# Performance work log

Measured on AMD Instinct MI355X. Metric: run time of the kernel, lower is better.

The kernel has to match this reference:

```python
import jax, jax.numpy as jnp
import numpy as np

N0, N1, N2 = 100000, 25000, 6250
E0, E1, E2 = 600000, 150000, 37500
K = 6


def cheb_conv(x, edge_index, W, b):
    """torch_geometric ChebConv with sym normalization, lambda_max=2:
    L_hat = -D^{-1/2} A D^{-1/2}; T0=x, T1=L_hat x, Tk=2 L_hat T_{k-1} - T_{k-2}."""
    n = x.shape[0]
    src, dst = edge_index[0], edge_index[1]
    deg = jax.ops.segment_sum(jnp.ones(src.shape[0], x.dtype), src, num_segments=n)
    dinv = jnp.where(deg > 0, jax.lax.rsqrt(jnp.maximum(deg, 1.0)), 0.0)
    w = -(dinv[src] * dinv[dst])  # [E]

    def prop(h):  # (L_hat h)_i = sum_{j->i} w_ij h_j
        return jax.ops.segment_sum(w[:, None] * h[src], dst, num_segments=n)

    Tx0 = x
    out = Tx0 @ W[0]
    Tx1 = prop(x)
    out = out + Tx1 @ W[1]
    for k in range(2, W.shape[0]):
        Tx2 = 2.0 * prop(Tx1) - Tx0
        out = out + Tx2 @ W[k]
        Tx0, Tx1 = Tx1, Tx2
    return out + b


def pool(x, rows, cols, vals, n_out):
    # sparse.mm(D, x): y[r] += v * x[c]
    return jax.ops.segment_sum(vals[:, None] * x[cols], rows, num_segments=n_out)


def setup_inputs() -> dict:
    key = jax.random.key(0)
    ks = jax.random.split(key, 16)
    inp = {}
    inp["x"] = jax.random.normal(ks[0], (N0, 3), jnp.float32)
    inp["edge_index0"] = jax.random.randint(ks[1], (2, E0), 0, N0, jnp.int32)
    inp["edge_index1"] = jax.random.randint(ks[2], (2, E1), 0, N1, jnp.int32)
    inp["edge_index2"] = jax.random.randint(ks[3], (2, E2), 0, N2, jnp.int32)
    s = 0.05
    inp["W0"] = jax.random.normal(ks[4], (K, 3, 128), jnp.float32) * s
    inp["b0"] = jax.random.normal(ks[5], (128,), jnp.float32) * s
    inp["W1"] = jax.random.normal(ks[6], (K, 128, 128), jnp.float32) * s
    inp["b1"] = jax.random.normal(ks[7], (128,), jnp.float32) * s
    inp["W2"] = jax.random.normal(ks[8], (K, 128, 256), jnp.float32) * s
    inp["b2"] = jax.random.normal(ks[9], (256,), jnp.float32) * s
    inp["D0_rows"] = jax.random.randint(ks[10], (100000,), 0, N1, jnp.int32)
    inp["D0_cols"] = jax.random.randint(ks[11], (100000,), 0, N0, jnp.int32)
    inp["D0_vals"] = jax.random.uniform(ks[12], (100000,), jnp.float32)
    inp["D1_rows"] = jax.random.randint(ks[13], (25000,), 0, N2, jnp.int32)
    inp["D1_cols"] = jax.random.randint(ks[14], (25000,), 0, N1, jnp.int32)
    inp["D1_vals"] = jax.random.uniform(ks[15], (25000,), jnp.float32)
    k2 = jax.random.split(jax.random.fold_in(key, 1), 2)
    inp["linW"] = jax.random.normal(k2[0], (10, N2 * 256), jnp.float32) * 0.001
    inp["linb"] = jax.random.normal(k2[1], (10,), jnp.float32) * s
    return inp


def reference(x, edge_index0, edge_index1, edge_index2, W0, b0, W1, b1, W2, b2,
              D0_rows, D0_cols, D0_vals, D1_rows, D1_cols, D1_vals, linW, linb):
    h = jax.nn.relu(cheb_conv(x, edge_index0, W0, b0))      # [N0,128]
    h = pool(h, D0_rows, D0_cols, D0_vals, N1)               # [N1,128]
    h = jax.nn.relu(cheb_conv(h, edge_index1, W1, b1))      # [N1,128]
    h = pool(h, D1_rows, D1_cols, D1_vals, N2)               # [N2,128]
    h = cheb_conv(h, edge_index2, W2, b2)                    # [N2,256]
    Z = linW @ h.reshape(-1) + linb                           # [10]
    return Z
```

## Files before the change

kernel.cpp:

```cpp
#include <hip/hip_runtime.h>


namespace {
constexpr int cN0 = 100000, cN1 = 25000, cN2 = 6250;
constexpr int cE0 = 600000, cE1 = 150000, cE2 = 37500;
constexpr int cD  = cN2 * 256;

constexpr int JN[8]  = {cN0, cN1, cN2, cN1, cN2, cN0, cN1, cN2};
constexpr int JE[8]  = {cE0, cE1, cE2, 100000, 25000, cE0, cE1, cE2};
constexpr int JB[8]  = {391, 98, 25, 98, 25, 391, 98, 25};
constexpr int JBBASE[9] = {0, 391, 489, 514, 612, 637, 1028, 1126, 1151};
constexpr int TB = 1151;
constexpr int JCB[8] = {293, 74, 19, 49, 13, 293, 74, 19};
constexpr int JCBASE[9] = {0, 293, 367, 386, 435, 448, 741, 815, 834};
constexpr int TCB = 834;
constexpr int CHUNK = 2048;
constexpr int BSTRIDE = 400;

constexpr int EBASE[5]   = {0, 600000, 750000, 787500, 887500};
constexpr int E_TOTAL    = 912500;
constexpr int SBASE[3]   = {0, 600000, 750000};
constexpr int S_TOTAL    = 787500;
constexpr int NBASE[5]   = {0, 100096, 125184, 131584, 156672};
constexpr int NPAD_TOTAL = 163072;
constexpr int DEGBASE[3] = {0, 100000, 125000};
constexpr int DEG_TOTAL  = 131250;
}

typedef __attribute__((ext_vector_type(8))) short short8;
typedef __attribute__((ext_vector_type(4))) float floatx4;

__device__ inline ushort f2bf(float f) {
  union { float f; unsigned u; } v; v.f = f;
  unsigned u = v.u;
  return (ushort)((u + 0x7FFFu + ((u >> 16) & 1u)) >> 16);
}

__device__ inline int job_of_cb(int cb) {
  int j = 0;
  while (cb >= JCBASE[j + 1]) ++j;
  return j;
}
__device__ inline int job_of_bucket(int g) {
  int j = 0;
  while (g >= JBBASE[j + 1]) ++j;
  return j;
}

__global__ __launch_bounds__(256) void c1_count_kernel(
    const int* __restrict__ k0, const int* __restrict__ k1, const int* __restrict__ k2,
    const int* __restrict__ k3, const int* __restrict__ k4, const int* __restrict__ k5,
    const int* __restrict__ k6, const int* __restrict__ k7,
    int* __restrict__ cntCB) {
  __shared__ int cnt[BSTRIDE];
  int cb = blockIdx.x;
  int j = job_of_cb(cb);
  int lb = cb - JCBASE[j];
  const int* keys;
  switch (j) {
    case 0: keys = k0; break; case 1: keys = k1; break; case 2: keys = k2; break;
    case 3: keys = k3; break; case 4: keys = k4; break; case 5: keys = k5; break;
    case 6: keys = k6; break; default: keys = k7; break;
  }
  int nB = JB[j];
  for (int b = threadIdx.x; b < nB; b += 256) cnt[b] = 0;
  __syncthreads();
  int e0 = lb * CHUNK;
  int e1 = min(e0 + CHUNK, JE[j]);
  for (int e = e0 + threadIdx.x; e < e1; e += 256)
    atomicAdd(&cnt[keys[e] >> 8], 1);
  __syncthreads();
  for (int b = threadIdx.x; b < nB; b += 256)
    cntCB[cb * BSTRIDE + b] = cnt[b];
}

__global__ __launch_bounds__(256) void c2a_scan_kernel(int* __restrict__ cntCB,
                                                       int* __restrict__ bucketTot) {
  __shared__ int s[256];
  int g = blockIdx.x;
  int j = job_of_bucket(g);
  int b = g - JBBASE[j];
  int cb0 = JCBASE[j], nCB = JCB[j];
  int carry = 0;
  for (int c0 = 0; c0 < nCB; c0 += 256) {
    int i = c0 + threadIdx.x;
    int v = (i < nCB) ? cntCB[(cb0 + i) * BSTRIDE + b] : 0;
    s[threadIdx.x] = v;
    __syncthreads();
    for (int d = 1; d < 256; d <<= 1) {
      int t = (threadIdx.x >= d) ? s[threadIdx.x - d] : 0;
      __syncthreads();
      s[threadIdx.x] += t;
      __syncthreads();
    }
    if (i < nCB) cntCB[(cb0 + i) * BSTRIDE + b] = carry + s[threadIdx.x] - v;
    carry += s[255];
    __syncthreads();
  }
  if (threadIdx.x == 0) bucketTot[g] = carry;
}

__global__ __launch_bounds__(256) void c2b_scan_kernel(const int* __restrict__ bucketTot,
                                                       int* __restrict__ bucketBase) {
  __shared__ int s[256];
  int j = blockIdx.x;
  int g0 = JBBASE[j], nB = JB[j];
  int carry = 0;
  for (int c0 = 0; c0 < nB; c0 += 256) {
    int i = c0 + threadIdx.x;
    int v = (i < nB) ? bucketTot[g0 + i] : 0;
    s[threadIdx.x] = v;
    __syncthreads();
    for (int d = 1; d < 256; d <<= 1) {
      int t = (threadIdx.x >= d) ? s[threadIdx.x - d] : 0;
      __syncthreads();
      s[threadIdx.x] += t;
      __syncthreads();
    }
    if (i < nB) bucketBase[g0 + i] = carry + s[threadIdx.x] - v;
    carry += s[255];
    __syncthreads();
  }
}

__global__ __launch_bounds__(256) void c3_src_kernel(
    const int* __restrict__ s0, const int* __restrict__ s1, const int* __restrict__ s2,
    const int* __restrict__ cntCB, const int* __restrict__ bucketBase,
    int* __restrict__ scatSrc) {
  __shared__ int base[BSTRIDE];
  int cb = blockIdx.x + JCBASE[5];
  int j = job_of_cb(cb);
  int lb = cb - JCBASE[j];
  const int* keys = (j == 5) ? s0 : (j == 6) ? s1 : s2;
  int nB = JB[j];
  for (int b = threadIdx.x; b < nB; b += 256)
    base[b] = SBASE[j - 5] + bucketBase[JBBASE[j] + b] + cntCB[cb * BSTRIDE + b];
  __syncthreads();
  int e0 = lb * CHUNK;
  int e1 = min(e0 + CHUNK, JE[j]);
  for (int e = e0 + threadIdx.x; e < e1; e += 256) {
    int s = keys[e];
    int pos = atomicAdd(&base[s >> 8], 1);
    scatSrc[pos] = s & 255;
  }
}

__global__ __launch_bounds__(256) void ddeg_kernel(const int* __restrict__ scatSrc,
                                                   const int* __restrict__ bucketTot,
                                                   const int* __restrict__ bucketBase,
                                                   float* __restrict__ dinv) {
  __shared__ int cnt[256];
  int g = blockIdx.x + JBBASE[5];
  int j = job_of_bucket(g);
  int b = g - JBBASE[j];
  int st = SBASE[j - 5] + bucketBase[g];
  int en = st + bucketTot[g];
  cnt[threadIdx.x] = 0;
  __syncthreads();
  for (int idx = st + threadIdx.x; idx < en; idx += 256)
    atomicAdd(&cnt[scatSrc[idx]], 1);
  __syncthreads();
  int node = b * 256 + threadIdx.x;
  if (node < JN[j]) {
    int c = cnt[threadIdx.x];
    dinv[DEGBASE[j - 5] + node] = (c > 0) ? rsqrtf((float)c) : 0.f;
  }
}

__global__ __launch_bounds__(256) void c3_dst_kernel(
    const int* __restrict__ d0, const int* __restrict__ s0,
    const int* __restrict__ d1, const int* __restrict__ s1,
    const int* __restrict__ d2, const int* __restrict__ s2,
    const int* __restrict__ p0r, const int* __restrict__ p0c, const float* __restrict__ p0v,
    const int* __restrict__ p1r, const int* __restrict__ p1c, const float* __restrict__ p1v,
    const float* __restrict__ dinv,
    const int* __restrict__ cntCB, const int* __restrict__ bucketBase,
    int2* __restrict__ scatPairs) {
  __shared__ int base[BSTRIDE];
  int cb = blockIdx.x;
  int j = job_of_cb(cb);
  int lb = cb - JCBASE[j];
  const int* dk; const int* sk; const float* vv = nullptr;
  switch (j) {
    case 0: dk = d0; sk = s0; break;
    case 1: dk = d1; sk = s1; break;
    case 2: dk = d2; sk = s2; break;
    case 3: dk = p0r; sk = p0c; vv = p0v; break;
    default: dk = p1r; sk = p1c; vv = p1v; break;
  }
  int nB = JB[j];
  for (int b = threadIdx.x; b < nB; b += 256)
    base[b] = EBASE[j] + bucketBase[JBBASE[j] + b] + cntCB[cb * BSTRIDE + b];
  __syncthreads();
  int e0 = lb * CHUNK;
  int e1 = min(e0 + CHUNK, JE[j]);
  for (int e = e0 + threadIdx.x; e < e1; e += 256) {
    int d = dk[e];
    int s = sk[e];
    float w;
    if (j < 3) w = -(dinv[DEGBASE[j] + s] * dinv[DEGBASE[j] + d]);
    else w = vv[e];
    int pos = atomicAdd(&base[d >> 8], 1);
    scatPairs[pos] = make_int2(((d & 255) << 17) | s, __float_as_int(w));
  }
}

__global__ __launch_bounds__(256) void dcsr_kernel(const int2* __restrict__ scatPairs,
                                                   const int* __restrict__ bucketTot,
                                                   const int* __restrict__ bucketBase,
                                                   int* __restrict__ off,
                                                   int2* __restrict__ csrPairs) {
  __shared__ int cnt[256];
  __shared__ int sArr[256];
  __shared__ int cur[256];
  int g = blockIdx.x;
  int j = job_of_bucket(g);
  int b = g - JBBASE[j];
  int relBase = bucketBase[g];
  int st = EBASE[j] + relBase;
  int en = st + bucketTot[g];
  cnt[threadIdx.x] = 0;
  __syncthreads();
  for (int idx = st + threadIdx.x; idx < en; idx += 256)
    atomicAdd(&cnt[scatPairs[idx].x >> 17], 1);
  __syncthreads();
  int v = cnt[threadIdx.x];
  sArr[threadIdx.x] = v;
  __syncthreads();
  for (int d = 1; d < 256; d <<= 1) {
    int t = (threadIdx.x >= d) ? sArr[threadIdx.x - d] : 0;
    __syncthreads();
    sArr[threadIdx.x] += t;
    __syncthreads();
  }
  int excl = sArr[threadIdx.x] - v;
  int node = b * 256 + threadIdx.x;
  if (node < JN[j]) off[NBASE[j] + node] = relBase + excl;
  if (threadIdx.x == 0 && b == JB[j] - 1) off[NBASE[j] + JN[j]] = JE[j];
  cur[threadIdx.x] = st + excl;
  __syncthreads();
  for (int idx = st + threadIdx.x; idx < en; idx += 256) {
    int2 p = scatPairs[idx];
    int dl = p.x >> 17;
    int s = p.x & 0x1FFFF;
    int pos = atomicAdd(&cur[dl], 1);
    csrPairs[pos] = make_int2(s, p.y);
  }
}

__global__ __launch_bounds__(256) void csr_prop128_kernel(
    const int* __restrict__ off, const int2* __restrict__ pairs,
    const float* __restrict__ h, float* __restrict__ y, ushort* __restrict__ ybf,
    const float* __restrict__ prev, float scale, int N) {
  int r = blockIdx.x * 8 + (threadIdx.x >> 5);
  int l = threadIdx.x & 31;
  if (r >= N) return;
  int s = off[r], e = off[r + 1];
  const float4* h4 = (const float4*)h;
  float ax = 0.f, ay = 0.f, az = 0.f, aw = 0.f;
  int j = s;
  for (; j + 4 <= e; j += 4) {
    int2 p0 = pairs[j], p1 = pairs[j + 1], p2 = pairs[j + 2], p3 = pairs[j + 3];
    float4 v0 = h4[(size_t)p0.x * 32 + l];
    float4 v1 = h4[(size_t)p1.x * 32 + l];
    float4 v2 = h4[(size_t)p2.x * 32 + l];
    float4 v3 = h4[(size_t)p3.x * 32 + l];
    float w0 = __int_as_float(p0.y), w1 = __int_as_float(p1.y);
    float w2 = __int_as_float(p2.y), w3 = __int_as_float(p3.y);
    ax += w0 * v0.x + w1 * v1.x + w2 * v2.x + w3 * v3.x;
    ay += w0 * v0.y + w1 * v1.y + w2 * v2.y + w3 * v3.y;
    az += w0 * v0.z + w1 * v1.z + w2 * v2.z + w3 * v3.z;
    aw += w0 * v0.w + w1 * v1.w + w2 * v2.w + w3 * v3.w;
  }
  for (; j < e; ++j) {
    int2 p = pairs[j];
    float4 v0 = h4[(size_t)p.x * 32 + l];
    float w = __int_as_float(p.y);
    ax += w * v0.x; ay += w * v0.y; az += w * v0.z; aw += w * v0.w;
  }
  float4 v = make_float4(scale * ax, scale * ay, scale * az, scale * aw);
  if (prev) {
    float4 pv = ((const float4*)prev)[(size_t)r * 32 + l];
    v.x -= pv.x; v.y -= pv.y; v.z -= pv.z; v.w -= pv.w;
  }
  if (y) ((float4*)y)[(size_t)r * 32 + l] = v;
  uint2 sp = make_uint2(f2bf(v.x) | ((unsigned)f2bf(v.y) << 16),
                        f2bf(v.z) | ((unsigned)f2bf(v.w) << 16));
  ((uint2*)ybf)[(size_t)r * 32 + l] = sp;
}

__global__ void csr_prop3_kernel(const int* __restrict__ off, const int2* __restrict__ pairs,
                                 const float4* __restrict__ h, float4* __restrict__ y,
                                 const float4* __restrict__ prev, float scale, int N) {
  int r = blockIdx.x * blockDim.x + threadIdx.x;
  if (r >= N) return;
  int s = off[r], e = off[r + 1];
  float ax = 0.f, ay = 0.f, az = 0.f;
  int j = s;
  for (; j + 4 <= e; j += 4) {
    int2 p0 = pairs[j], p1 = pairs[j + 1], p2 = pairs[j + 2], p3 = pairs[j + 3];
    float4 h0 = h[p0.x], h1 = h[p1.x], h2 = h[p2.x], h3 = h[p3.x];
    float w0 = __int_as_float(p0.y), w1 = __int_as_float(p1.y);
    float w2 = __int_as_float(p2.y), w3 = __int_as_float(p3.y);
    ax += w0 * h0.x + w1 * h1.x + w2 * h2.x + w3 * h3.x;
    ay += w0 * h0.y + w1 * h1.y + w2 * h2.y + w3 * h3.y;
    az += w0 * h0.z + w1 * h1.z + w2 * h2.z + w3 * h3.z;
  }
  for (; j < e; ++j) {
    int2 p = pairs[j];
    float4 hv = h[p.x];
    float w = __int_as_float(p.y);
    ax += w * hv.x; ay += w * hv.y; az += w * hv.z;
  }
  float4 v = make_float4(scale * ax, scale * ay, scale * az, 0.f);
  if (prev) {
    float4 pv = prev[r];
    v.x -= pv.x; v.y -= pv.y; v.z -= pv.z;
  }
  y[r] = v;
}

__global__ void copyx_kernel(const float* __restrict__ x, float4* __restrict__ Tb, int N) {
  int r = blockIdx.x * 256 + threadIdx.x;
  if (r < N) Tb[r] = make_float4(x[3 * r], x[3 * r + 1], x[3 * r + 2], 0.f);
}

__global__ __launch_bounds__(256) void h0_kernel(
    const float4* __restrict__ Tb0, const float* __restrict__ W0,
    const float* __restrict__ b0, float* __restrict__ h0, int N0) {
  int r = blockIdx.x * 2 + (threadIdx.x >> 7);
  int f = threadIdx.x & 127;
  float wcol[18];
#pragma unroll
  for (int t = 0; t < 18; ++t) wcol[t] = W0[t * 128 + f];
  if (r >= N0) return;
  float d = b0[f];
#pragma unroll
  for (int k = 0; k < 6; ++k) {
    float4 t = Tb0[(size_t)k * N0 + r];
    d += t.x * wcol[k * 3] + t.y * wcol[k * 3 + 1] + t.z * wcol[k * 3 + 2];
  }
  h0[(size_t)r * 128 + f] = fmaxf(d, 0.f);
}

__global__ void prep_w_kernel(const float* __restrict__ W1, const float* __restrict__ W2,
                              ushort* __restrict__ Wt1, ushort* __restrict__ Wt2) {
  int i = blockIdx.x * 256 + threadIdx.x;
  if (i < 768 * 128) {
    int k = i / 128, n = i - k * 128;
    Wt1[(size_t)n * 768 + k] = f2bf(W1[i]);
  } else {
    int i2 = i - 768 * 128;
    if (i2 < 768 * 256) {
      int k = i2 / 256, n = i2 - k * 256;
      Wt2[(size_t)n * 768 + k] = f2bf(W2[i2]);
    }
  }
}

template <int RELU>
__global__ __launch_bounds__(256, 2) void gemm_mfma_kernel(
    const ushort* __restrict__ Tbf, const ushort* __restrict__ Wt,
    const float* __restrict__ bias, float* __restrict__ C, int M, int N) {
  __shared__ ushort Al[64][40];
  __shared__ ushort Bl[128][40];
  const int tid = threadIdx.x;
  const int rowBase = blockIdx.x * 64;
  const int colBase = blockIdx.y * 128;
  const int wave = tid >> 6;
  const int lane = tid & 63;
  const int m16 = lane & 15;
  const int quad = lane >> 4;
  const size_t Mstride = (size_t)M * 128;

  floatx4 acc[8];
#pragma unroll
  for (int c = 0; c < 8; ++c)
#pragma unroll
    for (int r = 0; r < 4; ++r) acc[c][r] = 0.f;

  const int sRow = tid >> 2;
  const int sK8 = (tid & 3) * 8;
  const int growA = rowBase + sRow;
  const bool aValid = growA < M;

  for (int kc = 0; kc < 24; ++kc) {
    uint4 av = make_uint4(0, 0, 0, 0);
    if (aValid)
      av = *(const uint4*)(Tbf + (size_t)(kc >> 2) * Mstride + (size_t)growA * 128
                           + ((kc & 3) << 5) + sK8);
    *(uint4*)&Al[sRow][sK8] = av;
#pragma unroll
    for (int l = 0; l < 2; ++l) {
      int lin = tid + l * 256;
      int bRow = lin >> 2;
      int bK8 = (lin & 3) * 8;
      *(uint4*)&Bl[bRow][bK8] =
          *(const uint4*)(Wt + (size_t)(colBase + bRow) * 768 + kc * 32 + bK8);
    }
    __syncthreads();

    short8 a = *(const short8*)&Al[wave * 16 + m16][quad * 8];
#pragma unroll
    for (int c = 0; c < 8; ++c) {
      short8 b = *(const short8*)&Bl[c * 16 + m16][quad * 8];
      acc[c] = __builtin_amdgcn_mfma_f32_16x16x32_bf16(a, b, acc[c], 0, 0, 0);
    }
    __syncthreads();
  }

#pragma unroll
  for (int c = 0; c < 8; ++c) {
    int col = colBase + c * 16 + m16;
    float bv = bias[col];
#pragma unroll
    for (int r = 0; r < 4; ++r) {
      int row = rowBase + wave * 16 + quad * 4 + r;
      if (row < M) {
        float v = acc[c][r] + bv;
        if (RELU) v = fmaxf(v, 0.f);
        C[(size_t)row * N + col] = v;
      }
    }
  }
}

__global__ void initout_kernel(float* __restrict__ out, const float* __restrict__ linb) {
  int i = threadIdx.x;
  if (i < 10) out[i] = linb[i];
}

__global__ __launch_bounds__(256) void linear_kernel(const float* __restrict__ Wl,
                                                     const float* __restrict__ h,
                                                     float* __restrict__ out, int D) {
  float p[10];
#pragma unroll
  for (int j = 0; j < 10; ++j) p[j] = 0.f;
  int stride = gridDim.x * blockDim.x;
  for (int i = blockIdx.x * blockDim.x + threadIdx.x; i < D; i += stride) {
    float hv = h[i];
#pragma unroll
    for (int j = 0; j < 10; ++j) p[j] += Wl[(size_t)j * D + i] * hv;
  }
#pragma unroll
  for (int j = 0; j < 10; ++j) {
#pragma unroll
    for (int off = 32; off > 0; off >>= 1) p[j] += __shfl_down(p[j], off, 64);
  }
  __shared__ float s[4][10];
  int wave = threadIdx.x >> 6, lane = threadIdx.x & 63;
  if (lane == 0) {
#pragma unroll
    for (int j = 0; j < 10; ++j) s[wave][j] = p[j];
  }
  __syncthreads();
  if (threadIdx.x < 10) {
    float t = s[0][threadIdx.x] + s[1][threadIdx.x] + s[2][threadIdx.x] + s[3][threadIdx.x];
    atomicAdd(&out[threadIdx.x], t);
  }
}

extern "C" void kernel_launch(void* const* d_in, const int* in_sizes, int n_in,
                              void* d_out, int out_size, void* d_ws, size_t ws_size,
                              hipStream_t stream) {
  const float* x    = (const float*)d_in[0];
  const int*   ei0  = (const int*)d_in[1];
  const int*   ei1  = (const int*)d_in[2];
  const int*   ei2  = (const int*)d_in[3];
  const float* W0   = (const float*)d_in[4];
  const float* b0   = (const float*)d_in[5];
  const float* W1   = (const float*)d_in[6];
  const float* b1   = (const float*)d_in[7];
  const float* W2   = (const float*)d_in[8];
  const float* b2   = (const float*)d_in[9];
  const int*   D0r  = (const int*)d_in[10];
  const int*   D0c  = (const int*)d_in[11];
  const float* D0v  = (const float*)d_in[12];
  const int*   D1r  = (const int*)d_in[13];
  const int*   D1c  = (const int*)d_in[14];
  const float* D1v  = (const float*)d_in[15];
  const float* linW = (const float*)d_in[16];
  const float* linb = (const float*)d_in[17];
  float* out = (float*)d_out;
  (void)in_sizes; (void)n_in; (void)out_size; (void)ws_size;

  const int* src0 = ei0;            const int* dst0 = ei0 + cE0;
  const int* src1 = ei1;            const int* dst1 = ei1 + cE1;
  const int* src2 = ei2;            const int* dst2 = ei2 + cE2;

  float* ws = (float*)d_ws;
  size_t off = 0;
  auto alloc = [&](size_t n) {
    float* p = ws + off;
    off += (n + 63) & ~size_t(63);
    return p;
  };
  float* dinv       = alloc(DEG_TOTAL);
  int*   cntCB      = (int*)alloc((size_t)TCB * BSTRIDE);
  int*   bucketTot  = (int*)alloc(TB);
  int*   bucketBase = (int*)alloc(TB);
  int*   scatSrc    = (int*)alloc(S_TOTAL);
  int2*  scatPairs  = (int2*)alloc((size_t)2 * E_TOTAL);
  int2*  csrPairs   = (int2*)alloc((size_t)2 * E_TOTAL);
  int*   offArr     = (int*)alloc(NPAD_TOTAL);
  ushort* Wt1       = (ushort*)alloc(768 * 128 / 2);
  ushort* Wt2       = (ushort*)alloc(768 * 256 / 2);
  float4* Tb0       = (float4*)alloc((size_t)6 * cN0 * 4);
  float* h0buf      = alloc((size_t)cN0 * 128);
  float* Tlvl1      = alloc((size_t)6 * cN1 * 128);
  ushort* Tbf1      = (ushort*)alloc((size_t)6 * cN1 * 64);
  float* out1       = alloc((size_t)cN1 * 128);
  float* Tlvl2      = alloc((size_t)6 * cN2 * 128);
  ushort* Tbf2      = (ushort*)alloc((size_t)6 * cN2 * 64);
  float* out2       = alloc((size_t)cN2 * 256);

  auto nb = [](long long n) { return (unsigned)((n + 255) / 256); };

  c1_count_kernel<<<TCB, 256, 0, stream>>>(dst0, dst1, dst2, D0r, D1r,
                                           src0, src1, src2, cntCB);
  c2a_scan_kernel<<<TB, 256, 0, stream>>>(cntCB, bucketTot);
  c2b_scan_kernel<<<8, 256, 0, stream>>>(bucketTot, bucketBase);
  c3_src_kernel<<<TCB - JCBASE[5], 256, 0, stream>>>(src0, src1, src2,
                                                     cntCB, bucketBase, scatSrc);
  ddeg_kernel<<<TB - JBBASE[5], 256, 0, stream>>>(scatSrc, bucketTot, bucketBase, dinv);
  c3_dst_kernel<<<JCBASE[5], 256, 0, stream>>>(dst0, src0, dst1, src1, dst2, src2,
                                               D0r, D0c, D0v, D1r, D1c, D1v,
                                               dinv, cntCB, bucketBase, scatPairs);
  dcsr_kernel<<<JBBASE[5], 256, 0, stream>>>(scatPairs, bucketTot, bucketBase,
                                             offArr, csrPairs);
  prep_w_kernel<<<nb(768 * 384), 256, 0, stream>>>(W1, W2, Wt1, Wt2);

  auto seg_off   = [&](int s) { return offArr + NBASE[s]; };
  auto seg_pairs = [&](int s) { return csrPairs + EBASE[s]; };

  copyx_kernel<<<nb(cN0), 256, 0, stream>>>(x, Tb0, cN0);
  {
    auto Tk = [&](int k) { return Tb0 + (size_t)k * cN0; };
    csr_prop3_kernel<<<nb(cN0), 256, 0, stream>>>(seg_off(0), seg_pairs(0),
        Tk(0), Tk(1), nullptr, 1.f, cN0);
    csr_prop3_kernel<<<nb(cN0), 256, 0, stream>>>(seg_off(0), seg_pairs(0),
        Tk(1), Tk(2), Tk(0), 2.f, cN0);
    csr_prop3_kernel<<<nb(cN0), 256, 0, stream>>>(seg_off(0), seg_pairs(0),
        Tk(2), Tk(3), Tk(1), 2.f, cN0);
    csr_prop3_kernel<<<nb(cN0), 256, 0, stream>>>(seg_off(0), seg_pairs(0),
        Tk(3), Tk(4), Tk(2), 2.f, cN0);
    csr_prop3_kernel<<<nb(cN0), 256, 0, stream>>>(seg_off(0), seg_pairs(0),
        Tk(4), Tk(5), Tk(3), 2.f, cN0);
  }
  h0_kernel<<<(cN0 + 1) / 2, 256, 0, stream>>>(Tb0, W0, b0, h0buf, cN0);
  csr_prop128_kernel<<<(cN1 + 7) / 8, 256, 0, stream>>>(
      seg_off(3), seg_pairs(3), h0buf, Tlvl1, Tbf1, nullptr, 1.f, cN1);

  {
    auto Tk  = [&](int k) { return Tlvl1 + (size_t)k * cN1 * 128; };
    auto Tbk = [&](int k) { return Tbf1 + (size_t)k * cN1 * 128; };
    auto prop = [&](int kin, int kout, int kprev, float scale, bool needF32) {
      csr_prop128_kernel<<<(cN1 + 7) / 8, 256, 0, stream>>>(
          seg_off(1), seg_pairs(1), Tk(kin), needF32 ? Tk(kout) : nullptr, Tbk(kout),
          (kprev >= 0) ? Tk(kprev) : nullptr, scale, cN1);
    };
    prop(0, 1, -1, 1.f, true);
    prop(1, 2, 0, 2.f, true);
    prop(2, 3, 1, 2.f, true);
    prop(3, 4, 2, 2.f, true);
    prop(4, 5, 3, 2.f, false);
    dim3 g((cN1 + 63) / 64, 1);
    gemm_mfma_kernel<1><<<g, 256, 0, stream>>>(Tbf1, Wt1, b1, out1, cN1, 128);
  }

  csr_prop128_kernel<<<(cN2 + 7) / 8, 256, 0, stream>>>(
      seg_off(4), seg_pairs(4), out1, Tlvl2, Tbf2, nullptr, 1.f, cN2);

  {
    auto Tk  = [&](int k) { return Tlvl2 + (size_t)k * cN2 * 128; };
    auto Tbk = [&](int k) { return Tbf2 + (size_t)k * cN2 * 128; };
    auto prop = [&](int kin, int kout, int kprev, float scale, bool needF32) {
      csr_prop128_kernel<<<(cN2 + 7) / 8, 256, 0, stream>>>(
          seg_off(2), seg_pairs(2), Tk(kin), needF32 ? Tk(kout) : nullptr, Tbk(kout),
          (kprev >= 0) ? Tk(kprev) : nullptr, scale, cN2);
    };
    prop(0, 1, -1, 1.f, true);
    prop(1, 2, 0, 2.f, true);
    prop(2, 3, 1, 2.f, true);
    prop(3, 4, 2, 2.f, true);
    prop(4, 5, 3, 2.f, false);
    dim3 g((cN2 + 63) / 64, 2);
    gemm_mfma_kernel<0><<<g, 256, 0, stream>>>(Tbf2, Wt2, b2, out2, cN2, 256);
  }

  initout_kernel<<<1, 64, 0, stream>>>(out, linb);
  linear_kernel<<<512, 256, 0, stream>>>(linW, out2, out, cD);
}
```

Measured before the change: 481.2 us.

## Compute level-0 Chebyshev projection with bf16 MFMA instead of scalar FMA

The Chebyshev terms for the 3-channel input are now also written into a packed bf16 [N0,32] buffer, using 4 slots per order with padding. The level-0 dense projection runs as one 16x16x32 bf16 MFMA per output tile instead of a per-thread scalar dot product over 18 weights. This targets the compute and launch cost of the old h0 kernel, which used 50k blocks. In exchange it adds extra bf16 stores in the propagation kernels and lowers the projection's precision to bf16.

```diff
diff --git a/kernel.cpp b/kernel.cpp
--- a/kernel.cpp
+++ b/kernel.cpp
@@ -291,7 +291,8 @@
 
 __global__ void csr_prop3_kernel(const int* __restrict__ off, const int2* __restrict__ pairs,
                                  const float4* __restrict__ h, float4* __restrict__ y,
-                                 const float4* __restrict__ prev, float scale, int N) {
+                                 const float4* __restrict__ prev, float scale, int N,
+                                 ushort* __restrict__ ybf, int kout) {
   int r = blockIdx.x * blockDim.x + threadIdx.x;
   if (r >= N) return;
   int s = off[r], e = off[r + 1];
@@ -318,42 +319,88 @@
     v.x -= pv.x; v.y -= pv.y; v.z -= pv.z;
   }
   y[r] = v;
-}
-
-__global__ void copyx_kernel(const float* __restrict__ x, float4* __restrict__ Tb, int N) {
+  uint2 sp = make_uint2(f2bf(v.x) | ((unsigned)f2bf(v.y) << 16), (unsigned)f2bf(v.z));
+  *(uint2*)(ybf + (size_t)r * 32 + kout * 4) = sp;
+}
+
+__global__ void copyx_kernel(const float* __restrict__ x, float4* __restrict__ Tb,
+                             ushort* __restrict__ Abf, int N) {
   int r = blockIdx.x * 256 + threadIdx.x;
-  if (r < N) Tb[r] = make_float4(x[3 * r], x[3 * r + 1], x[3 * r + 2], 0.f);
-}
-
-__global__ __launch_bounds__(256) void h0_kernel(
-    const float4* __restrict__ Tb0, const float* __restrict__ W0,
-    const float* __restrict__ b0, float* __restrict__ h0, int N0) {
-  int r = blockIdx.x * 2 + (threadIdx.x >> 7);
-  int f = threadIdx.x & 127;
-  float wcol[18];
-#pragma unroll
-  for (int t = 0; t < 18; ++t) wcol[t] = W0[t * 128 + f];
-  if (r >= N0) return;
-  float d = b0[f];
-#pragma unroll
-  for (int k = 0; k < 6; ++k) {
-    float4 t = Tb0[(size_t)k * N0 + r];
-    d += t.x * wcol[k * 3] + t.y * wcol[k * 3 + 1] + t.z * wcol[k * 3 + 2];
-  }
-  h0[(size_t)r * 128 + f] = fmaxf(d, 0.f);
-}
-
-__global__ void prep_w_kernel(const float* __restrict__ W1, const float* __restrict__ W2,
+  if (r >= N) return;
+  float x0 = x[3 * r], x1 = x[3 * r + 1], x2 = x[3 * r + 2];
+  Tb[r] = make_float4(x0, x1, x2, 0.f);
+  uint4 z = make_uint4(0, 0, 0, 0);
+  uint4 first = make_uint4(f2bf(x0) | ((unsigned)f2bf(x1) << 16), (unsigned)f2bf(x2), 0, 0);
+  uint4* p = (uint4*)(Abf + (size_t)r * 32);
+  p[0] = first; p[1] = z; p[2] = z; p[3] = z;
+}
+
+__global__ __launch_bounds__(256, 2) void h0_mfma_kernel(
+    const ushort* __restrict__ Abf, const ushort* __restrict__ W0b,
+    const float* __restrict__ b0, float* __restrict__ h0, int M) {
+  __shared__ ushort Al[64][40];
+  __shared__ ushort Bl[128][40];
+  const int tid = threadIdx.x;
+  const int rowBase = blockIdx.x * 64;
+  const int wave = tid >> 6;
+  const int lane = tid & 63;
+  const int m16 = lane & 15;
+  const int quad = lane >> 4;
+  {
+    int sRow = tid >> 2;
+    int sK8 = (tid & 3) * 8;
+    int row = rowBase + sRow;
+    uint4 av = make_uint4(0, 0, 0, 0);
+    if (row < M) av = *(const uint4*)(Abf + (size_t)row * 32 + sK8);
+    *(uint4*)&Al[sRow][sK8] = av;
+  }
+#pragma unroll
+  for (int l = 0; l < 2; ++l) {
+    int lin = tid + l * 256;
+    int bRow = lin >> 2;
+    int bK8 = (lin & 3) * 8;
+    *(uint4*)&Bl[bRow][bK8] = *(const uint4*)(W0b + (size_t)bRow * 32 + bK8);
+  }
+  __syncthreads();
+  short8 a = *(const short8*)&Al[wave * 16 + m16][quad * 8];
+  floatx4 acc[8];
+#pragma unroll
+  for (int c = 0; c < 8; ++c) {
+    floatx4 z;
+    z[0] = 0.f; z[1] = 0.f; z[2] = 0.f; z[3] = 0.f;
+    short8 b = *(const short8*)&Bl[c * 16 + m16][quad * 8];
+    acc[c] = __builtin_amdgcn_mfma_f32_16x16x32_bf16(a, b, z, 0, 0, 0);
+  }
+#pragma unroll
+  for (int c = 0; c < 8; ++c) {
+    int col = c * 16 + m16;
+    float bv = b0[col];
+#pragma unroll
+    for (int r = 0; r < 4; ++r) {
+      int row = rowBase + wave * 16 + quad * 4 + r;
+      if (row < M) h0[(size_t)row * 128 + col] = fmaxf(acc[c][r] + bv, 0.f);
+    }
+  }
+}
+
+__global__ void prep_w_kernel(const float* __restrict__ W0, const float* __restrict__ W1,
+                              const float* __restrict__ W2, ushort* __restrict__ W0b,
                               ushort* __restrict__ Wt1, ushort* __restrict__ Wt2) {
   int i = blockIdx.x * 256 + threadIdx.x;
   if (i < 768 * 128) {
     int k = i / 128, n = i - k * 128;
     Wt1[(size_t)n * 768 + k] = f2bf(W1[i]);
+  } else if (i < 768 * 128 + 768 * 256) {
+    int i2 = i - 768 * 128;
+    int k = i2 / 256, n = i2 - k * 256;
+    Wt2[(size_t)n * 768 + k] = f2bf(W2[i2]);
   } else {
-    int i2 = i - 768 * 128;
-    if (i2 < 768 * 256) {
-      int k = i2 / 256, n = i2 - k * 256;
-      Wt2[(size_t)n * 768 + k] = f2bf(W2[i2]);
+    int i3 = i - 768 * 128 - 768 * 256;
+    if (i3 < 128 * 32) {
+      int col = i3 >> 5, k = i3 & 31;
+      int a = k >> 2, jj = k & 3;
+      float v = (k < 24 && jj < 3) ? W0[(a * 3 + jj) * 128 + col] : 0.f;
+      W0b[(size_t)col * 32 + k] = f2bf(v);
     }
   }
 }
@@ -503,9 +550,11 @@
   int2*  scatPairs  = (int2*)alloc((size_t)2 * E_TOTAL);
   int2*  csrPairs   = (int2*)alloc((size_t)2 * E_TOTAL);
   int*   offArr     = (int*)alloc(NPAD_TOTAL);
+  ushort* W0b       = (ushort*)alloc(128 * 32 / 2);
   ushort* Wt1       = (ushort*)alloc(768 * 128 / 2);
   ushort* Wt2       = (ushort*)alloc(768 * 256 / 2);
   float4* Tb0       = (float4*)alloc((size_t)6 * cN0 * 4);
+  ushort* Abf0      = (ushort*)alloc((size_t)cN0 * 16);
   float* h0buf      = alloc((size_t)cN0 * 128);
   float* Tlvl1      = alloc((size_t)6 * cN1 * 128);
   ushort* Tbf1      = (ushort*)alloc((size_t)6 * cN1 * 64);
@@ -528,26 +577,26 @@
                                                dinv, cntCB, bucketBase, scatPairs);
   dcsr_kernel<<<JBBASE[5], 256, 0, stream>>>(scatPairs, bucketTot, bucketBase,
                                              offArr, csrPairs);
-  prep_w_kernel<<<nb(768 * 384), 256, 0, stream>>>(W1, W2, Wt1, Wt2);
+  prep_w_kernel<<<nb(768 * 384 + 128 * 32), 256, 0, stream>>>(W0, W1, W2, W0b, Wt1, Wt2);
 
   auto seg_off   = [&](int s) { return offArr + NBASE[s]; };
   auto seg_pairs = [&](int s) { return csrPairs + EBASE[s]; };
 
-  copyx_kernel<<<nb(cN0), 256, 0, stream>>>(x, Tb0, cN0);
+  copyx_kernel<<<nb(cN0), 256, 0, stream>>>(x, Tb0, Abf0, cN0);
   {
     auto Tk = [&](int k) { return Tb0 + (size_t)k * cN0; };
     csr_prop3_kernel<<<nb(cN0), 256, 0, stream>>>(seg_off(0), seg_pairs(0),
-        Tk(0), Tk(1), nullptr, 1.f, cN0);
+        Tk(0), Tk(1), nullptr, 1.f, cN0, Abf0, 1);
     csr_prop3_kernel<<<nb(cN0), 256, 0, stream>>>(seg_off(0), seg_pairs(0),
-        Tk(1), Tk(2), Tk(0), 2.f, cN0);
+        Tk(1), Tk(2), Tk(0), 2.f, cN0, Abf0, 2);
     csr_prop3_kernel<<<nb(cN0), 256, 0, stream>>>(seg_off(0), seg_pairs(0),
-        Tk(2), Tk(3), Tk(1), 2.f, cN0);
+        Tk(2), Tk(3), Tk(1), 2.f, cN0, Abf0, 3);
     csr_prop3_kernel<<<nb(cN0), 256, 0, stream>>>(seg_off(0), seg_pairs(0),
-        Tk(3), Tk(4), Tk(2), 2.f, cN0);
+        Tk(3), Tk(4), Tk(2), 2.f, cN0, Abf0, 4);
     csr_prop3_kernel<<<nb(cN0), 256, 0, stream>>>(seg_off(0), seg_pairs(0),
-        Tk(4), Tk(5), Tk(3), 2.f, cN0);
-  }
-  h0_kernel<<<(cN0 + 1) / 2, 256, 0, stream>>>(Tb0, W0, b0, h0buf, cN0);
+        Tk(4), Tk(5), Tk(3), 2.f, cN0, Abf0, 5);
+  }
+  h0_mfma_kernel<<<(cN0 + 63) / 64, 256, 0, stream>>>(Abf0, W0b, b0, h0buf, cN0);
   csr_prop128_kernel<<<(cN1 + 7) / 8, 256, 0, stream>>>(
       seg_off(3), seg_pairs(3), h0buf, Tlvl1, Tbf1, nullptr, 1.f, cN1);
 
```

New measurement: 433.7 us. 9.9% less time.
